# Kernel tuning notes

Measured on AMD Instinct MI355X. Metric: run time of the kernel, lower is better.

## Reference

```python
import jax, jax.numpy as jnp
import numpy as np

B, L, D = 8, 4096, 512  # batch, seq_len (power of 2), in_features
R_MIN, R_MAX = 0.9, 0.999


def setup_inputs() -> dict:
    key = jax.random.key(0)
    k1, k2, k3 = jax.random.split(key, 3)
    inputs = jax.random.normal(k1, (B, L, D), dtype=jnp.float32)
    # Linear layers: i_dense D->2D, o_dense 2D->D (torch Linear: y = x @ W.T + b)
    Wi = jax.random.normal(k2, (2 * D, D), dtype=jnp.float32) / np.sqrt(D)
    bi = jnp.zeros((2 * D,), dtype=jnp.float32)
    Wo = jax.random.normal(k3, (D, 2 * D), dtype=jnp.float32) / np.sqrt(2 * D)
    bo = jnp.zeros((D,), dtype=jnp.float32)
    # LRU param init, exactly as in the torch module
    rng = np.random.RandomState(0)
    u1 = rng.random_sample(D)
    u2 = rng.random_sample(D)
    v_log = np.log(-0.5 * np.log(u1 * (R_MAX ** 2 - R_MIN ** 2) + R_MIN ** 2))
    theta_log = np.log(u2 * np.pi * 2)
    gamma_log = np.log(np.sqrt(1 - np.exp(-np.exp(v_log)) ** 2))
    params_log = jnp.asarray(np.stack([v_log, theta_log, gamma_log]), dtype=jnp.float32)
    return {"inputs": inputs, "Wi": Wi, "bi": bi, "Wo": Wo, "bo": bo,
            "params_log": params_log}


def reference(inputs, Wi, bi, Wo, bo, params_log):
    b, lin, d = inputs.shape
    u = inputs @ Wi.T + bi                       # [B, L, 2D]
    params = jnp.exp(params_log)                 # [3, D]
    v, theta, gamma = params[0], params[1], params[2]
    log2_L = int(np.ceil(np.log2(lin)))
    Lp = 2 ** log2_L
    # interleaved (real, imag) pairs -> complex state
    u = u.reshape(b, lin, d, 2)
    x = jax.lax.complex(u[..., 0], u[..., 1])    # [B, L, D] complex64
    if Lp > lin:
        x = jnp.pad(x, ((0, 0), (0, Lp - lin), (0, 0)))
    # Blelloch-style doubling scan: after stage i, each block of length 2^i
    # holds the prefix-scanned values x_t = lam*x_{t-1} + u_t within the block.
    for i in range(1, log2_L + 1):
        l = 2 ** i
        xr = x.reshape(b * Lp // l, l, d)
        x1, x2 = xr[:, : l // 2], xr[:, l // 2 :]
        pos = jnp.arange(1, l // 2 + 1, dtype=jnp.float32)        # [l/2]
        lambs = jnp.exp(jax.lax.complex(-pos[:, None] * v,
                                        pos[:, None] * theta))   # [l/2, D]
        x2 = x2 + lambs * x1[:, -1:]
        x = jnp.concatenate([x1, x2], axis=1).reshape(b, Lp, d)
    x = x[:, :lin] * gamma.astype(jnp.complex64)
    xr = jnp.concatenate([jnp.real(x), jnp.imag(x)], axis=-1)     # [B, L, 2D]
    out = xr @ Wo.T + bo
    return jax.nn.relu(out)
```

## Files before the change

kernel.cpp:

```cpp
#include <hip/hip_runtime.h>
#include <cstdint>
#include <cstddef>

typedef unsigned short u16;
typedef unsigned int   u32;

typedef short bf16x8 __attribute__((ext_vector_type(8)));
typedef float f32x4  __attribute__((ext_vector_type(4)));

__device__ __forceinline__ u16 f2bf(float f) {
  u32 u = __float_as_uint(f);
  u += 0x7fffu + ((u >> 16) & 1u);
  return (u16)(u >> 16);
}
__device__ __forceinline__ float bflo(u32 w) { return __uint_as_float((w & 0xffffu) << 16); }
__device__ __forceinline__ float bfhi(u32 w) { return __uint_as_float(w & 0xffff0000u); }

#define GLB_AS(p) ((const __attribute__((address_space(1))) void*)(p))
#define LDS_AS(p) ((__attribute__((address_space(3))) void*)(p))

__global__ __launch_bounds__(256) void conv_f32_bf16(const float* __restrict__ src,
                                                     u16* __restrict__ dst, int n4) {
  int i = blockIdx.x * 256 + threadIdx.x;
  if (i >= n4) return;
  float4 v = ((const float4*)src)[i];
  u32 lo = (u32)f2bf(v.x) | ((u32)f2bf(v.y) << 16);
  u32 hi = (u32)f2bf(v.z) | ((u32)f2bf(v.w) << 16);
  ((uint2*)dst)[i] = make_uint2(lo, hi);
}

template<int OUT_BF16, int RELU>
__global__ __launch_bounds__(256)
void gemm_bt(const u16* __restrict__ A, const u16* __restrict__ Bw,
             const float* __restrict__ bias, void* __restrict__ Cout,
             int M, int N, int K)
{
  __shared__ __align__(16) u16 As[128 * 32];
  __shared__ __align__(16) u16 Bs[128 * 32];

  const int tid  = threadIdx.x;
  const int lane = tid & 63;
  const int wave = tid >> 6;
  const int m0 = blockIdx.x * 128;
  const int n0 = blockIdx.y * 128;
  const int wm = (wave & 1) * 64;
  const int wn = (wave >> 1) * 64;

  f32x4 acc[4][4];
#pragma unroll
  for (int i = 0; i < 4; ++i)
#pragma unroll
    for (int j = 0; j < 4; ++j) acc[i][j] = f32x4{0.f, 0.f, 0.f, 0.f};

  const int g0 = tid;
  const int g1 = 256 + tid;
  const int r0 = g0 >> 2, c0 = (((g0 & 3) ^ (r0 & 3)) << 3);
  const int r1 = g1 >> 2, c1 = (((g1 & 3) ^ (r1 & 3)) << 3);
  const u16* Asrc0 = A  + (size_t)(m0 + r0) * K + c0;
  const u16* Asrc1 = A  + (size_t)(m0 + r1) * K + c1;
  const u16* Bsrc0 = Bw + (size_t)(n0 + r0) * K + c0;
  const u16* Bsrc1 = Bw + (size_t)(n0 + r1) * K + c1;
  u16* ldsA0 = &As[(0 * 256 + wave * 64) * 8];
  u16* ldsA1 = &As[(1 * 256 + wave * 64) * 8];
  u16* ldsB0 = &Bs[(0 * 256 + wave * 64) * 8];
  u16* ldsB1 = &Bs[(1 * 256 + wave * 64) * 8];

  const int fm = lane & 15;
  const int q  = lane >> 4;
  int aoff[4], boff[4];
#pragma unroll
  for (int i = 0; i < 4; ++i) {
    int ml = wm + i * 16 + fm;
    aoff[i] = (ml * 4 + (q ^ (ml & 3))) * 8;
    int nl = wn + i * 16 + fm;
    boff[i] = (nl * 4 + (q ^ (nl & 3))) * 8;
  }

  for (int k0 = 0; k0 < K; k0 += 32) {
    __builtin_amdgcn_global_load_lds(GLB_AS(Asrc0 + k0), LDS_AS(ldsA0), 16, 0, 0);
    __builtin_amdgcn_global_load_lds(GLB_AS(Asrc1 + k0), LDS_AS(ldsA1), 16, 0, 0);
    __builtin_amdgcn_global_load_lds(GLB_AS(Bsrc0 + k0), LDS_AS(ldsB0), 16, 0, 0);
    __builtin_amdgcn_global_load_lds(GLB_AS(Bsrc1 + k0), LDS_AS(ldsB1), 16, 0, 0);
    __syncthreads();

    bf16x8 af[4], bfr[4];
#pragma unroll
    for (int i = 0; i < 4; ++i) af[i]  = *(const bf16x8*)&As[aoff[i]];
#pragma unroll
    for (int i = 0; i < 4; ++i) bfr[i] = *(const bf16x8*)&Bs[boff[i]];
#pragma unroll
    for (int mi = 0; mi < 4; ++mi)
#pragma unroll
      for (int ni = 0; ni < 4; ++ni)
        acc[mi][ni] = __builtin_amdgcn_mfma_f32_16x16x32_bf16(af[mi], bfr[ni],
                                                              acc[mi][ni], 0, 0, 0);
    __syncthreads();
  }

  const int colL = lane & 15;
  const int rowQ = (lane >> 4) * 4;
#pragma unroll
  for (int mi = 0; mi < 4; ++mi) {
#pragma unroll
    for (int ni = 0; ni < 4; ++ni) {
      int col  = n0 + wn + ni * 16 + colL;
      int rowb = m0 + wm + mi * 16 + rowQ;
      float bv = bias[col];
#pragma unroll
      for (int r = 0; r < 4; ++r) {
        float v = acc[mi][ni][r] + bv;
        if (RELU) v = fmaxf(v, 0.f);
        size_t idx = (size_t)(rowb + r) * N + col;
        if (OUT_BF16) ((u16*)Cout)[idx] = f2bf(v);
        else          ((float*)Cout)[idx] = v;
      }
    }
  }
}

__global__ __launch_bounds__(512)
void scan_chunk_end(const u16* __restrict__ u, const float* __restrict__ plog,
                    float2* __restrict__ e)
{
  const int j = threadIdx.x;
  const int c = blockIdx.x;
  const int b = blockIdx.y;
  float vv  = expf(plog[j]);
  float th  = expf(plog[512 + j]);
  float mag = expf(-vv);
  float lr = mag * cosf(th), li = mag * sinf(th);
  const u32* up = (const u32*)u;
  size_t idx = (size_t)(b * 4096 + c * 128) * 512 + j;
  float hr = 0.f, hi = 0.f;
#pragma unroll 8
  for (int t = 0; t < 128; ++t) {
    u32 w = up[idx]; idx += 512;
    float ur = bflo(w), ui = bfhi(w);
    float nr = fmaf(lr, hr, fmaf(-li, hi, ur));
    float ni2 = fmaf(lr, hi, fmaf(li, hr, ui));
    hr = nr; hi = ni2;
  }
  e[(size_t)(b * 32 + c) * 512 + j] = make_float2(hr, hi);
}

__global__ __launch_bounds__(512)
void scan_carry(const float2* __restrict__ e, const float* __restrict__ plog,
                float2* __restrict__ carry)
{
  const int j = threadIdx.x;
  const int b = blockIdx.x;
  float vv = expf(plog[j]);
  float th = expf(plog[512 + j]);
  float mag = expf(-128.f * vv);
  float a = 128.f * th;
  float lr = mag * cosf(a), li = mag * sinf(a);
  float Hr = 0.f, Hi = 0.f;
  for (int c = 0; c < 32; ++c) {
    size_t o = (size_t)(b * 32 + c) * 512 + j;
    carry[o] = make_float2(Hr, Hi);
    float2 ec = e[o];
    float nr = fmaf(lr, Hr, fmaf(-li, Hi, ec.x));
    float ni2 = fmaf(lr, Hi, fmaf(li, Hr, ec.y));
    Hr = nr; Hi = ni2;
  }
}

__global__ __launch_bounds__(512)
void scan_out(const u16* __restrict__ u, const float* __restrict__ plog,
              const float2* __restrict__ carry, u16* __restrict__ xr)
{
  const int j = threadIdx.x;
  const int c = blockIdx.x;
  const int b = blockIdx.y;
  float vv  = expf(plog[j]);
  float th  = expf(plog[512 + j]);
  float gm  = expf(plog[1024 + j]);
  float mag = expf(-vv);
  float lr = mag * cosf(th), li = mag * sinf(th);
  float2 h0 = carry[(size_t)(b * 32 + c) * 512 + j];
  float hr = h0.x, hi = h0.y;
  const u32* up = (const u32*)u;
  size_t uidx = (size_t)(b * 4096 + c * 128) * 512 + j;
  size_t xidx = (size_t)(b * 4096 + c * 128) * 1024 + j;
#pragma unroll 4
  for (int t = 0; t < 128; ++t) {
    u32 w = up[uidx]; uidx += 512;
    float ur = bflo(w), ui = bfhi(w);
    float nr = fmaf(lr, hr, fmaf(-li, hi, ur));
    float ni2 = fmaf(lr, hi, fmaf(li, hr, ui));
    hr = nr; hi = ni2;
    xr[xidx]       = f2bf(gm * hr);
    xr[xidx + 512] = f2bf(gm * hi);
    xidx += 1024;
  }
}

extern "C" void kernel_launch(void* const* d_in, const int* in_sizes, int n_in,
                              void* d_out, int out_size, void* d_ws, size_t ws_size,
                              hipStream_t stream)
{
  (void)in_sizes; (void)n_in; (void)out_size; (void)ws_size;
  const float* inputs = (const float*)d_in[0];
  const float* Wi     = (const float*)d_in[1];
  const float* bi     = (const float*)d_in[2];
  const float* Wo     = (const float*)d_in[3];
  const float* bo     = (const float*)d_in[4];
  const float* plog   = (const float*)d_in[5];

  char* ws = (char*)d_ws;
  u16*    xrA   = (u16*)(ws);
  u16*    u_bf  = (u16*)(ws + 67108864ull);
  u16*    Wi_bf = (u16*)(ws + 134217728ull);
  u16*    Wo_bf = (u16*)(ws + 135266304ull);
  float2* e_b   = (float2*)(ws + 136314880ull);
  float2* ca_b  = (float2*)(ws + 137363456ull);

  conv_f32_bf16<<<16384, 256, 0, stream>>>(inputs, xrA, 4194304);
  conv_f32_bf16<<<512,   256, 0, stream>>>(Wi, Wi_bf, 131072);
  conv_f32_bf16<<<512,   256, 0, stream>>>(Wo, Wo_bf, 131072);

  gemm_bt<1, 0><<<dim3(256, 8), 256, 0, stream>>>(xrA, Wi_bf, bi, u_bf,
                                                  32768, 1024, 512);

  scan_chunk_end<<<dim3(32, 8), 512, 0, stream>>>(u_bf, plog, e_b);
  scan_carry<<<8, 512, 0, stream>>>(e_b, plog, ca_b);
  scan_out<<<dim3(32, 8), 512, 0, stream>>>(u_bf, plog, ca_b, xrA);

  gemm_bt<0, 1><<<dim3(256, 4), 256, 0, stream>>>(xrA, Wo_bf, bo, d_out,
                                                  32768, 512, 1024);
}
```

Measured before the change: 286.1 us.

## Fuse conversions, use single-wave double-buffered GEMM, fold carry scan into output

Merges the three fp32->bf16 conversion launches into one kernel. Replaces the 4-wave 128x128 GEMM with a single-wave 64x64 tile that double-buffers LDS, issuing the next k-slice with async global->LDS loads while computing the current one under explicit vmcnt waits. Removes the separate carry kernel: each scan_out block recomputes its prefix carry from the chunk-end values. This cuts launches and adds load/compute overlap, at the cost of lower per-block reuse in the GEMM and redundant serial carry work in later chunks.

```diff
diff --git a/kernel.cpp b/kernel.cpp
--- a/kernel.cpp
+++ b/kernel.cpp
@@ -19,10 +19,16 @@
 #define GLB_AS(p) ((const __attribute__((address_space(1))) void*)(p))
 #define LDS_AS(p) ((__attribute__((address_space(3))) void*)(p))
 
-__global__ __launch_bounds__(256) void conv_f32_bf16(const float* __restrict__ src,
-                                                     u16* __restrict__ dst, int n4) {
-  int i = blockIdx.x * 256 + threadIdx.x;
-  if (i >= n4) return;
+__global__ __launch_bounds__(256)
+void conv3_f32_bf16(const float* __restrict__ in, u16* __restrict__ a,
+                    const float* __restrict__ wi, u16* __restrict__ wib,
+                    const float* __restrict__ wo, u16* __restrict__ wob)
+{
+  long i = (long)blockIdx.x * 256 + threadIdx.x;
+  const float* src; u16* dst;
+  if (i < 4194304L) { src = in; dst = a; }
+  else if (i < 4325376L) { i -= 4194304L; src = wi; dst = wib; }
+  else { i -= 4325376L; if (i >= 131072L) return; src = wo; dst = wob; }
   float4 v = ((const float4*)src)[i];
   u32 lo = (u32)f2bf(v.x) | ((u32)f2bf(v.y) << 16);
   u32 hi = (u32)f2bf(v.z) | ((u32)f2bf(v.w) << 16);
@@ -30,21 +36,18 @@
 }
 
 template<int OUT_BF16, int RELU>
-__global__ __launch_bounds__(256)
-void gemm_bt(const u16* __restrict__ A, const u16* __restrict__ Bw,
+__global__ __launch_bounds__(64)
+void gemm_wt(const u16* __restrict__ A, const u16* __restrict__ Bw,
              const float* __restrict__ bias, void* __restrict__ Cout,
-             int M, int N, int K)
-{
-  __shared__ __align__(16) u16 As[128 * 32];
-  __shared__ __align__(16) u16 Bs[128 * 32];
-
-  const int tid  = threadIdx.x;
-  const int lane = tid & 63;
-  const int wave = tid >> 6;
-  const int m0 = blockIdx.x * 128;
-  const int n0 = blockIdx.y * 128;
-  const int wm = (wave & 1) * 64;
-  const int wn = (wave >> 1) * 64;
+             int M, int N, int K, int lognb)
+{
+  __shared__ __align__(16) u16 As[2][64 * 32];
+  __shared__ __align__(16) u16 Bs[2][64 * 32];
+
+  const int lane = threadIdx.x;
+  const int bid  = blockIdx.x;
+  const int m0 = (bid >> lognb) * 64;
+  const int n0 = (bid & ((1 << lognb) - 1)) * 64;
 
   f32x4 acc[4][4];
 #pragma unroll
@@ -52,63 +55,88 @@
 #pragma unroll
     for (int j = 0; j < 4; ++j) acc[i][j] = f32x4{0.f, 0.f, 0.f, 0.f};
 
-  const int g0 = tid;
-  const int g1 = 256 + tid;
-  const int r0 = g0 >> 2, c0 = (((g0 & 3) ^ (r0 & 3)) << 3);
-  const int r1 = g1 >> 2, c1 = (((g1 & 3) ^ (r1 & 3)) << 3);
-  const u16* Asrc0 = A  + (size_t)(m0 + r0) * K + c0;
-  const u16* Asrc1 = A  + (size_t)(m0 + r1) * K + c1;
-  const u16* Bsrc0 = Bw + (size_t)(n0 + r0) * K + c0;
-  const u16* Bsrc1 = Bw + (size_t)(n0 + r1) * K + c1;
-  u16* ldsA0 = &As[(0 * 256 + wave * 64) * 8];
-  u16* ldsA1 = &As[(1 * 256 + wave * 64) * 8];
-  u16* ldsB0 = &Bs[(0 * 256 + wave * 64) * 8];
-  u16* ldsB1 = &Bs[(1 * 256 + wave * 64) * 8];
-
+  const u16* Ap[4]; const u16* Bp[4];
+#pragma unroll
+  for (int i = 0; i < 4; ++i) {
+    int g = i * 64 + lane;
+    int r = g >> 2;
+    int c = ((g & 3) ^ ((r >> 1) & 3)) << 3;
+    Ap[i] = A  + (size_t)(m0 + r) * K + c;
+    Bp[i] = Bw + (size_t)(n0 + r) * K + c;
+  }
   const int fm = lane & 15;
   const int q  = lane >> 4;
-  int aoff[4], boff[4];
+  int foff[4];
 #pragma unroll
   for (int i = 0; i < 4; ++i) {
-    int ml = wm + i * 16 + fm;
-    aoff[i] = (ml * 4 + (q ^ (ml & 3))) * 8;
-    int nl = wn + i * 16 + fm;
-    boff[i] = (nl * 4 + (q ^ (nl & 3))) * 8;
-  }
-
-  for (int k0 = 0; k0 < K; k0 += 32) {
-    __builtin_amdgcn_global_load_lds(GLB_AS(Asrc0 + k0), LDS_AS(ldsA0), 16, 0, 0);
-    __builtin_amdgcn_global_load_lds(GLB_AS(Asrc1 + k0), LDS_AS(ldsA1), 16, 0, 0);
-    __builtin_amdgcn_global_load_lds(GLB_AS(Bsrc0 + k0), LDS_AS(ldsB0), 16, 0, 0);
-    __builtin_amdgcn_global_load_lds(GLB_AS(Bsrc1 + k0), LDS_AS(ldsB1), 16, 0, 0);
-    __syncthreads();
-
-    bf16x8 af[4], bfr[4];
-#pragma unroll
-    for (int i = 0; i < 4; ++i) af[i]  = *(const bf16x8*)&As[aoff[i]];
-#pragma unroll
-    for (int i = 0; i < 4; ++i) bfr[i] = *(const bf16x8*)&Bs[boff[i]];
-#pragma unroll
-    for (int mi = 0; mi < 4; ++mi)
-#pragma unroll
-      for (int ni = 0; ni < 4; ++ni)
-        acc[mi][ni] = __builtin_amdgcn_mfma_f32_16x16x32_bf16(af[mi], bfr[ni],
-                                                              acc[mi][ni], 0, 0, 0);
-    __syncthreads();
+    int m = i * 16 + fm;
+    foff[i] = (m * 4 + (q ^ ((m >> 1) & 3))) * 8;
   }
 
   const int colL = lane & 15;
+  float bvv[4];
+#pragma unroll
+  for (int ni = 0; ni < 4; ++ni) bvv[ni] = bias[n0 + ni * 16 + colL];
+  asm volatile("s_waitcnt vmcnt(0)" ::: "memory");
+
+#define ISSUE_TILE(kk, buf)                                                        \
+  {                                                                                \
+    u16* la_ = &As[buf][0]; u16* lb_ = &Bs[buf][0];                                \
+    _Pragma("unroll")                                                              \
+    for (int i = 0; i < 4; ++i)                                                    \
+      __builtin_amdgcn_global_load_lds(GLB_AS(Ap[i] + (kk)), LDS_AS(la_ + i*512), 16, 0, 0); \
+    _Pragma("unroll")                                                              \
+    for (int i = 0; i < 4; ++i)                                                    \
+      __builtin_amdgcn_global_load_lds(GLB_AS(Bp[i] + (kk)), LDS_AS(lb_ + i*512), 16, 0, 0); \
+  }
+
+#define COMPUTE_TILE(buf)                                                          \
+  {                                                                                \
+    const u16* la_ = &As[buf][0]; const u16* lb_ = &Bs[buf][0];                    \
+    bf16x8 af[4], bf[4];                                                           \
+    _Pragma("unroll")                                                              \
+    for (int i = 0; i < 4; ++i) { af[i] = *(const bf16x8*)(la_ + foff[i]);         \
+                                  bf[i] = *(const bf16x8*)(lb_ + foff[i]); }       \
+    _Pragma("unroll")                                                              \
+    for (int mi = 0; mi < 4; ++mi)                                                 \
+      _Pragma("unroll")                                                            \
+      for (int ni = 0; ni < 4; ++ni)                                               \
+        acc[mi][ni] = __builtin_amdgcn_mfma_f32_16x16x32_bf16(af[mi], bf[ni],      \
+                                                              acc[mi][ni], 0, 0, 0); \
+  }
+
+  ISSUE_TILE(0, 0)
+  ISSUE_TILE(32, 1)
+
+  for (int kt = 0; kt < K; kt += 64) {
+    const bool more = (kt + 64) < K;
+    if (more) {
+      asm volatile("s_waitcnt vmcnt(8)" ::: "memory");
+      COMPUTE_TILE(0)
+      ISSUE_TILE(kt + 64, 0)
+      asm volatile("s_waitcnt vmcnt(8)" ::: "memory");
+      COMPUTE_TILE(1)
+      ISSUE_TILE(kt + 96, 1)
+    } else {
+      asm volatile("s_waitcnt vmcnt(8)" ::: "memory");
+      COMPUTE_TILE(0)
+      asm volatile("s_waitcnt vmcnt(0)" ::: "memory");
+      COMPUTE_TILE(1)
+    }
+  }
+#undef ISSUE_TILE
+#undef COMPUTE_TILE
+
   const int rowQ = (lane >> 4) * 4;
 #pragma unroll
   for (int mi = 0; mi < 4; ++mi) {
 #pragma unroll
     for (int ni = 0; ni < 4; ++ni) {
-      int col  = n0 + wn + ni * 16 + colL;
-      int rowb = m0 + wm + mi * 16 + rowQ;
-      float bv = bias[col];
+      int col  = n0 + ni * 16 + colL;
+      int rowb = m0 + mi * 16 + rowQ;
 #pragma unroll
       for (int r = 0; r < 4; ++r) {
-        float v = acc[mi][ni][r] + bv;
+        float v = acc[mi][ni][r] + bvv[ni];
         if (RELU) v = fmaxf(v, 0.f);
         size_t idx = (size_t)(rowb + r) * N + col;
         if (OUT_BF16) ((u16*)Cout)[idx] = f2bf(v);
@@ -144,30 +172,8 @@
 }
 
 __global__ __launch_bounds__(512)
-void scan_carry(const float2* __restrict__ e, const float* __restrict__ plog,
-                float2* __restrict__ carry)
-{
-  const int j = threadIdx.x;
-  const int b = blockIdx.x;
-  float vv = expf(plog[j]);
-  float th = expf(plog[512 + j]);
-  float mag = expf(-128.f * vv);
-  float a = 128.f * th;
-  float lr = mag * cosf(a), li = mag * sinf(a);
-  float Hr = 0.f, Hi = 0.f;
-  for (int c = 0; c < 32; ++c) {
-    size_t o = (size_t)(b * 32 + c) * 512 + j;
-    carry[o] = make_float2(Hr, Hi);
-    float2 ec = e[o];
-    float nr = fmaf(lr, Hr, fmaf(-li, Hi, ec.x));
-    float ni2 = fmaf(lr, Hi, fmaf(li, Hr, ec.y));
-    Hr = nr; Hi = ni2;
-  }
-}
-
-__global__ __launch_bounds__(512)
-void scan_out(const u16* __restrict__ u, const float* __restrict__ plog,
-              const float2* __restrict__ carry, u16* __restrict__ xr)
+void scan_out2(const u16* __restrict__ u, const float* __restrict__ plog,
+               const float2* __restrict__ e, u16* __restrict__ xr)
 {
   const int j = threadIdx.x;
   const int c = blockIdx.x;
@@ -177,8 +183,18 @@
   float gm  = expf(plog[1024 + j]);
   float mag = expf(-vv);
   float lr = mag * cosf(th), li = mag * sinf(th);
-  float2 h0 = carry[(size_t)(b * 32 + c) * 512 + j];
-  float hr = h0.x, hi = h0.y;
+
+  float Lm = expf(-128.f * vv);
+  float La = 128.f * th;
+  float Lr = Lm * cosf(La), Li = Lm * sinf(La);
+  float hr = 0.f, hi = 0.f;
+  for (int i = 0; i < c; ++i) {
+    float2 ec = e[(size_t)(b * 32 + i) * 512 + j];
+    float nr = fmaf(Lr, hr, fmaf(-Li, hi, ec.x));
+    float ni2 = fmaf(Lr, hi, fmaf(Li, hr, ec.y));
+    hr = nr; hi = ni2;
+  }
+
   const u32* up = (const u32*)u;
   size_t uidx = (size_t)(b * 4096 + c * 128) * 512 + j;
   size_t xidx = (size_t)(b * 4096 + c * 128) * 1024 + j;
@@ -213,19 +229,15 @@
   u16*    Wi_bf = (u16*)(ws + 134217728ull);
   u16*    Wo_bf = (u16*)(ws + 135266304ull);
   float2* e_b   = (float2*)(ws + 136314880ull);
-  float2* ca_b  = (float2*)(ws + 137363456ull);
-
-  conv_f32_bf16<<<16384, 256, 0, stream>>>(inputs, xrA, 4194304);
-  conv_f32_bf16<<<512,   256, 0, stream>>>(Wi, Wi_bf, 131072);
-  conv_f32_bf16<<<512,   256, 0, stream>>>(Wo, Wo_bf, 131072);
-
-  gemm_bt<1, 0><<<dim3(256, 8), 256, 0, stream>>>(xrA, Wi_bf, bi, u_bf,
-                                                  32768, 1024, 512);
+
+  conv3_f32_bf16<<<17408, 256, 0, stream>>>(inputs, xrA, Wi, Wi_bf, Wo, Wo_bf);
+
+  gemm_wt<1, 0><<<8192, 64, 0, stream>>>(xrA, Wi_bf, bi, u_bf,
+                                         32768, 1024, 512, 4);
 
   scan_chunk_end<<<dim3(32, 8), 512, 0, stream>>>(u_bf, plog, e_b);
-  scan_carry<<<8, 512, 0, stream>>>(e_b, plog, ca_b);
-  scan_out<<<dim3(32, 8), 512, 0, stream>>>(u_bf, plog, ca_b, xrA);
-
-  gemm_bt<0, 1><<<dim3(256, 4), 256, 0, stream>>>(xrA, Wo_bf, bo, d_out,
-                                                  32768, 512, 1024);
-}
+  scan_out2<<<dim3(32, 8), 512, 0, stream>>>(u_bf, plog, e_b, xrA);
+
+  gemm_wt<0, 1><<<4096, 64, 0, stream>>>(xrA, Wo_bf, bo, d_out,
+                                         32768, 512, 1024, 3);
+}
```

Measured after the change: 325.7 us. +13.9%, slower.
